# Performance work log

Hardware: AMD Instinct MI355X
Metric: run time of the kernel (lower is better)

The kernel has to match this reference:

```python
import jax, jax.numpy as jnp
import numpy as np

N = 100000
E = 1600000
C_IN = 32
HEADS = 4
C = 32          # per-head out channels
L = 3           # num layers = num_hidden_layers + 1
NEG_SLOPE = 0.2


def setup_inputs() -> dict:
    key = jax.random.key(0)
    ks = jax.random.split(key, 8)
    x = jax.random.normal(ks[0], (N, C_IN), dtype=jnp.float32)
    edge_index = jax.random.randint(ks[1], (2, E), 0, N, dtype=jnp.int64)
    edge_attr = jax.random.normal(ks[2], (E, 8), dtype=jnp.float32)  # unused by GATConv (edge_dim=None)
    scale = 1.0 / np.sqrt(C_IN)
    Ws = jax.random.normal(ks[3], (L, C_IN, HEADS * C), dtype=jnp.float32) * scale
    att_src = jax.random.normal(ks[4], (L, HEADS, C), dtype=jnp.float32) * scale
    att_dst = jax.random.normal(ks[5], (L, HEADS, C), dtype=jnp.float32) * scale
    bias = jnp.zeros((L, C), dtype=jnp.float32)
    return {"x": x, "edge_index": edge_index, "edge_attr": edge_attr,
            "Ws": Ws, "att_src": att_src, "att_dst": att_dst, "bias": bias}


def _gat_layer(x, src, dst, W, a_src, a_dst, b):
    # x: [N, C_in]; src/dst: [E'] (self-loops included); W: [C_in, H*C]
    h = (x @ W).reshape(N, HEADS, C)                      # [N, H, C]
    alpha_src = jnp.sum(h * a_src, axis=-1)               # [N, H]
    alpha_dst = jnp.sum(h * a_dst, axis=-1)               # [N, H]
    e = alpha_src[src] + alpha_dst[dst]                   # [E', H]
    e = jnp.where(e > 0, e, NEG_SLOPE * e)                # leaky_relu
    # segment softmax over incoming edges of each dst node
    m = jax.ops.segment_max(e, dst, num_segments=N)       # [N, H]
    ex = jnp.exp(e - m[dst])
    s = jax.ops.segment_sum(ex, dst, num_segments=N)      # [N, H]
    alpha = ex / (s[dst] + 1e-16)                         # [E', H]
    msg = h[src] * alpha[:, :, None]                      # [E', H, C]
    out = jax.ops.segment_sum(msg, dst, num_segments=N)   # [N, H, C]
    return out.mean(axis=1) + b                           # concat=False -> mean over heads, + bias


def reference(x, edge_index, edge_attr, Ws, att_src, att_dst, bias):
    # add self loops once (GATConv add_self_loops=True)
    loops = jnp.arange(N, dtype=edge_index.dtype)
    src = jnp.concatenate([edge_index[0], loops])
    dst = jnp.concatenate([edge_index[1], loops])
    # edge_attr unused: GATConv built without edge_dim.
    # Dropout layers are identity in eval mode.
    for l in range(L):
        x = _gat_layer(x, src, dst, Ws[l], att_src[l], att_dst[l], bias[l])
        x = jax.nn.elu(x)
    return x
```

## Files before the change

### kernel.cpp

```cpp
#include <hip/hip_runtime.h>
#include <hip/hip_bf16.h>
#include <hip/hip_fp16.h>
#include <cstdint>


__global__ void k_scan1(const int* __restrict__ deg, int n, int* __restrict__ bsums) {
    __shared__ int s[256];
    int t = threadIdx.x;
    int i = blockIdx.x * 256 + t;
    int v = (i < n) ? deg[i] : 0;
    s[t] = v; __syncthreads();
    for (int off = 128; off > 0; off >>= 1) {
        if (t < off) s[t] += s[t + off];
        __syncthreads();
    }
    if (t == 0) bsums[blockIdx.x] = s[0];
}

__global__ void k_scan2(const int* __restrict__ bsums, int nb, int* __restrict__ boffs) {
    __shared__ int s[512];
    int t = threadIdx.x;
    int v = (t < nb) ? bsums[t] : 0;
    s[t] = v; __syncthreads();
    for (int off = 1; off < 512; off <<= 1) {
        int nv = (t >= off) ? s[t - off] : 0;
        __syncthreads();
        s[t] += nv;
        __syncthreads();
    }
    if (t < nb) boffs[t] = s[t] - v;
}

__global__ void k_scan3(const int* __restrict__ deg, int n, const int* __restrict__ boffs,
                        int* __restrict__ rowst) {
    __shared__ int s[256];
    int t = threadIdx.x;
    int i = blockIdx.x * 256 + t;
    int v = (i < n) ? deg[i] : 0;
    s[t] = v; __syncthreads();
    for (int off = 1; off < 256; off <<= 1) {
        int nv = (t >= off) ? s[t - off] : 0;
        __syncthreads();
        s[t] += nv;
        __syncthreads();
    }
    int incl = s[t] + boffs[blockIdx.x];
    if (i < n) {
        rowst[i] = incl - v;
        if (i == n - 1) rowst[n] = incl;
    }
}

__global__ void k_scatter(const int* __restrict__ src, const int* __restrict__ dst,
                          const int* __restrict__ rank, const int* __restrict__ rowst,
                          int E, int* __restrict__ col) {
    int t = blockIdx.x * blockDim.x + threadIdx.x;
    int base = t * 8;
    if (base + 8 <= E) {
        int4 d[2], s[2], r[2];
#pragma unroll
        for (int k = 0; k < 2; ++k) {
            d[k] = *reinterpret_cast<const int4*>(dst + base + k * 4);
            s[k] = *reinterpret_cast<const int4*>(src + base + k * 4);
            r[k] = *reinterpret_cast<const int4*>(rank + base + k * 4);
        }
        const int* dd = reinterpret_cast<const int*>(d);
        const int* ss = reinterpret_cast<const int*>(s);
        const int* rr = reinterpret_cast<const int*>(r);
        int p[8];
#pragma unroll
        for (int k = 0; k < 8; ++k) p[k] = rowst[dd[k]] + rr[k];
#pragma unroll
        for (int k = 0; k < 8; ++k) col[p[k]] = ss[k];
    } else {
        for (int i = base; i < E; ++i) col[rowst[dst[i]] + rank[i]] = src[i];
    }
}


__device__ __forceinline__ float lane_bcast(float v, int k) {
    return __int_as_float(__builtin_amdgcn_readlane(__float_as_int(v), k));
}

__global__ void __launch_bounds__(256)
k_gemm_alpha(const float* __restrict__ x, const float* __restrict__ W,
             const float* __restrict__ a_src, const float* __restrict__ a_dst,
             __half* __restrict__ h16, float* __restrict__ alpha_src,
             float* __restrict__ alpha_dst, int n,
             const int* __restrict__ dstv, int E, int* __restrict__ deg,
             int* __restrict__ rank, int gemmBlocks) {
    if ((int)blockIdx.x >= gemmBlocks) {
        int b = blockIdx.x - gemmBlocks;
        int base = (b * 256 + threadIdx.x) * 8;
        if (base + 8 <= E) {
            int4 d[2];
#pragma unroll
            for (int k = 0; k < 2; ++k)
                d[k] = *reinterpret_cast<const int4*>(dstv + base + k * 4);
            const int* dd = reinterpret_cast<const int*>(d);
            int r[8];
#pragma unroll
            for (int k = 0; k < 8; ++k) r[k] = atomicAdd(&deg[dd[k]], 1);
#pragma unroll
            for (int k = 0; k < 2; ++k)
                *reinterpret_cast<int4*>(rank + base + k * 4) =
                    *reinterpret_cast<const int4*>(r + k * 4);
        } else {
            for (int i = base; i < E; ++i) rank[i] = atomicAdd(&deg[dstv[i]], 1);
        }
        return;
    }
    int lane = threadIdx.x & 63;
    int wave = threadIdx.x >> 6;
    int j2 = lane * 2;
    int nbase = blockIdx.x * 64 + wave * 16;

    float2 wr[32];
#pragma unroll
    for (int k = 0; k < 32; ++k)
        wr[k] = *reinterpret_cast<const float2*>(W + k * 128 + j2);
    float2 as2 = *reinterpret_cast<const float2*>(a_src + j2);
    float2 ad2 = *reinterpret_cast<const float2*>(a_dst + j2);

    float xr[16];
#pragma unroll
    for (int m = 0; m < 16; ++m) {
        int node = nbase + m;
        xr[m] = (node < n) ? x[(size_t)node * 32 + (lane & 31)] : 0.f;
    }

#pragma unroll
    for (int m = 0; m < 16; ++m) {
        int node = nbase + m;
        if (node >= n) continue;
        float acc0 = 0.f, acc1 = 0.f;
#pragma unroll
        for (int k = 0; k < 32; ++k) {
            float xv = lane_bcast(xr[m], k);
            acc0 += xv * wr[k].x;
            acc1 += xv * wr[k].y;
        }
        *reinterpret_cast<__half2*>(h16 + (size_t)node * 128 + j2) =
            __floats2half2_rn(acc0, acc1);
        float ps = acc0 * as2.x + acc1 * as2.y;
        float pd = acc0 * ad2.x + acc1 * ad2.y;
#pragma unroll
        for (int mm = 1; mm < 16; mm <<= 1) {
            ps += __shfl_xor(ps, mm, 64);
            pd += __shfl_xor(pd, mm, 64);
        }
        if ((lane & 15) == 0) {
            int head = lane >> 4;
            alpha_src[node * 4 + head] = ps;
            alpha_dst[node * 4 + head] = pd;
        }
    }
}

__device__ __forceinline__ float lrelu_exp(float e) {
    e = e > 0.f ? e : 0.2f * e;
    return __expf(e);
}

__device__ __forceinline__ float4 h16_to_f4(uint2 v) {
    float2 fa = __half22float2(*reinterpret_cast<__half2*>(&v.x));
    float2 fb = __half22float2(*reinterpret_cast<__half2*>(&v.y));
    return make_float4(fa.x, fa.y, fb.x, fb.y);
}

__global__ void k_agg(const __half* __restrict__ h16, const float* __restrict__ asrc,
                      const float* __restrict__ adst, const int* __restrict__ rowst,
                      const int* __restrict__ col, const float* __restrict__ bias,
                      float* __restrict__ out, int n) {
    int wid = (int)((blockIdx.x * (size_t)blockDim.x + threadIdx.x) >> 6);
    if (wid >= n) return;
    int lane = threadIdx.x & 63;
    int half = lane >> 5;
    int q = lane & 31;
    int head = q >> 3;
    float ad = adst[wid * 4 + head];

    float4 acc = make_float4(0.f, 0.f, 0.f, 0.f);
    float s = 0.f;
    if (half == 0) {
        float w = lrelu_exp(asrc[wid * 4 + head] + ad);
        uint2 v = *reinterpret_cast<const uint2*>(h16 + (size_t)wid * 128 + q * 4);
        float4 hv = h16_to_f4(v);
        s = w;
        acc.x = w * hv.x; acc.y = w * hv.y; acc.z = w * hv.z; acc.w = w * hv.w;
    }

    int beg = rowst[wid], end = rowst[wid + 1];
    int i = beg;
    for (; i + 8 <= end; i += 8) {
        int base = i + half * 4;
        int s0 = col[base], s1 = col[base + 1], s2 = col[base + 2], s3 = col[base + 3];
        float x0 = asrc[s0 * 4 + head];
        float x1 = asrc[s1 * 4 + head];
        float x2 = asrc[s2 * 4 + head];
        float x3 = asrc[s3 * 4 + head];
        uint2 v0 = *reinterpret_cast<const uint2*>(h16 + (size_t)s0 * 128 + q * 4);
        uint2 v1 = *reinterpret_cast<const uint2*>(h16 + (size_t)s1 * 128 + q * 4);
        uint2 v2 = *reinterpret_cast<const uint2*>(h16 + (size_t)s2 * 128 + q * 4);
        uint2 v3 = *reinterpret_cast<const uint2*>(h16 + (size_t)s3 * 128 + q * 4);
        float w0 = lrelu_exp(x0 + ad);
        float w1 = lrelu_exp(x1 + ad);
        float w2 = lrelu_exp(x2 + ad);
        float w3 = lrelu_exp(x3 + ad);
        float4 h0 = h16_to_f4(v0), h1 = h16_to_f4(v1), h2 = h16_to_f4(v2), h3 = h16_to_f4(v3);
        s += w0 + w1 + w2 + w3;
        acc.x += w0 * h0.x + w1 * h1.x + w2 * h2.x + w3 * h3.x;
        acc.y += w0 * h0.y + w1 * h1.y + w2 * h2.y + w3 * h3.y;
        acc.z += w0 * h0.z + w1 * h1.z + w2 * h2.z + w3 * h3.z;
        acc.w += w0 * h0.w + w1 * h1.w + w2 * h2.w + w3 * h3.w;
    }
    for (; i + 2 <= end; i += 2) {
        int sidx = col[i + half];
        float w = lrelu_exp(asrc[sidx * 4 + head] + ad);
        float4 hv = h16_to_f4(*reinterpret_cast<const uint2*>(h16 + (size_t)sidx * 128 + q * 4));
        s += w;
        acc.x += w * hv.x; acc.y += w * hv.y; acc.z += w * hv.z; acc.w += w * hv.w;
    }
    if (i < end && half == 0) {
        int sidx = col[i];
        float w = lrelu_exp(asrc[sidx * 4 + head] + ad);
        float4 hv = h16_to_f4(*reinterpret_cast<const uint2*>(h16 + (size_t)sidx * 128 + q * 4));
        s += w;
        acc.x += w * hv.x; acc.y += w * hv.y; acc.z += w * hv.z; acc.w += w * hv.w;
    }

    s += __shfl_xor(s, 32, 64);
    acc.x += __shfl_xor(acc.x, 32, 64);
    acc.y += __shfl_xor(acc.y, 32, 64);
    acc.z += __shfl_xor(acc.z, 32, 64);
    acc.w += __shfl_xor(acc.w, 32, 64);
    float inv = 1.f / s;
    acc.x *= inv; acc.y *= inv; acc.z *= inv; acc.w *= inv;
    acc.x += __shfl_xor(acc.x, 8, 64);  acc.x += __shfl_xor(acc.x, 16, 64);
    acc.y += __shfl_xor(acc.y, 8, 64);  acc.y += __shfl_xor(acc.y, 16, 64);
    acc.z += __shfl_xor(acc.z, 8, 64);  acc.z += __shfl_xor(acc.z, 16, 64);
    acc.w += __shfl_xor(acc.w, 8, 64);  acc.w += __shfl_xor(acc.w, 16, 64);
    if (lane < 8) {
        float4 b4 = *reinterpret_cast<const float4*>(&bias[lane * 4]);
        float o0 = acc.x * 0.25f + b4.x;
        float o1 = acc.y * 0.25f + b4.y;
        float o2 = acc.z * 0.25f + b4.z;
        float o3 = acc.w * 0.25f + b4.w;
        o0 = o0 > 0.f ? o0 : (__expf(o0) - 1.f);
        o1 = o1 > 0.f ? o1 : (__expf(o1) - 1.f);
        o2 = o2 > 0.f ? o2 : (__expf(o2) - 1.f);
        o3 = o3 > 0.f ? o3 : (__expf(o3) - 1.f);
        *reinterpret_cast<float4*>(&out[(size_t)wid * 32 + lane * 4]) =
            make_float4(o0, o1, o2, o3);
    }
}


extern "C" void kernel_launch(void* const* d_in, const int* in_sizes, int n_in,
                              void* d_out, int out_size, void* d_ws, size_t ws_size,
                              hipStream_t stream) {
    const float* x       = (const float*)d_in[0];
    const int*   ei      = (const int*)d_in[1];
    const float* Ws      = (const float*)d_in[3];
    const float* att_src = (const float*)d_in[4];
    const float* att_dst = (const float*)d_in[5];
    const float* bias    = (const float*)d_in[6];

    int N = in_sizes[0] / 32;
    int E = in_sizes[1] / 2;
    const int* srcv = ei;
    const int* dstv = ei + E;

    float* fws   = (float*)d_ws;
    __half* h16  = (__half*)fws;
    float* asrc  = (float*)(h16 + (size_t)N * 128);
    float* adst  = asrc + (size_t)N * 4;
    float* xbuf  = adst + (size_t)N * 4;
    int*   deg    = (int*)(xbuf + (size_t)N * 32);
    int*   rowst  = deg + N;
    int*   bsums  = rowst + N + 1;
    int*   boffs  = bsums + 512;
    int*   col    = boffs + 512;
    int*   rank   = col + E;

    int nb256 = (N + 255) / 256;
    int gemmBlocks = (N + 63) / 64;
    int edgeBlocks8 = (E + 8 * 256 - 1) / (8 * 256);

    hipMemsetAsync(deg, 0, (size_t)N * sizeof(int), stream);

    for (int l = 0; l < 3; ++l) {
        const float* xin = (l == 0) ? x : xbuf;
        float* xout = (l == 2) ? (float*)d_out : xbuf;
        int extra = (l == 0) ? edgeBlocks8 : 0;
        k_gemm_alpha<<<gemmBlocks + extra, 256, 0, stream>>>(
            xin, Ws + (size_t)l * 32 * 128, att_src + l * 128, att_dst + l * 128,
            h16, asrc, adst, N, dstv, E, deg, rank, gemmBlocks);
        if (l == 0) {
            k_scan1<<<nb256, 256, 0, stream>>>(deg, N, bsums);
            k_scan2<<<1, 512, 0, stream>>>(bsums, nb256, boffs);
            k_scan3<<<nb256, 256, 0, stream>>>(deg, N, boffs, rowst);
            k_scatter<<<edgeBlocks8, 256, 0, stream>>>(srcv, dstv, rank, rowst, E, col);
        }
        k_agg<<<(N + 3) / 4, 256, 0, stream>>>(
            h16, asrc, adst, rowst, col, bias + l * 32, xout, N);
    }
}
```

Baseline: 448.1 us.

## Replicate degree histogram across eight copies to spread atomic contention in CSR build

```diff
diff --git a/kernel.cpp b/kernel.cpp
--- a/kernel.cpp
+++ b/kernel.cpp
@@ -3,6 +3,21 @@
 #include <hip/hip_fp16.h>
 #include <cstdint>
 
+#define NREP 8
+
+
+__global__ void k_prefix(int* __restrict__ deg_r, int n, int* __restrict__ deg) {
+    int i = blockIdx.x * blockDim.x + threadIdx.x;
+    if (i >= n) return;
+    int sum = 0;
+#pragma unroll
+    for (int r = 0; r < NREP; ++r) {
+        int v = deg_r[r * n + i];
+        deg_r[r * n + i] = sum;
+        sum += v;
+    }
+    deg[i] = sum;
+}
 
 __global__ void k_scan1(const int* __restrict__ deg, int n, int* __restrict__ bsums) {
     __shared__ int s[256];
@@ -32,7 +47,7 @@
 }
 
 __global__ void k_scan3(const int* __restrict__ deg, int n, const int* __restrict__ boffs,
-                        int* __restrict__ rowst) {
+                        int* __restrict__ rowst, int* __restrict__ deg_r) {
     __shared__ int s[256];
     int t = threadIdx.x;
     int i = blockIdx.x * 256 + t;
@@ -46,14 +61,17 @@
     }
     int incl = s[t] + boffs[blockIdx.x];
     if (i < n) {
-        rowst[i] = incl - v;
+        int ex = incl - v;
+        rowst[i] = ex;
         if (i == n - 1) rowst[n] = incl;
+#pragma unroll
+        for (int r = 0; r < NREP; ++r) deg_r[r * n + i] += ex;
     }
 }
 
 __global__ void k_scatter(const int* __restrict__ src, const int* __restrict__ dst,
-                          const int* __restrict__ rank, const int* __restrict__ rowst,
-                          int E, int* __restrict__ col) {
+                          const int* __restrict__ rank, const int* __restrict__ deg_r,
+                          int n, int E, int* __restrict__ col) {
     int t = blockIdx.x * blockDim.x + threadIdx.x;
     int base = t * 8;
     if (base + 8 <= E) {
@@ -69,11 +87,15 @@
         const int* rr = reinterpret_cast<const int*>(r);
         int p[8];
 #pragma unroll
-        for (int k = 0; k < 8; ++k) p[k] = rowst[dd[k]] + rr[k];
+        for (int k = 0; k < 8; ++k)
+            p[k] = deg_r[(rr[k] & (NREP - 1)) * n + dd[k]] + (rr[k] >> 3);
 #pragma unroll
         for (int k = 0; k < 8; ++k) col[p[k]] = ss[k];
     } else {
-        for (int i = base; i < E; ++i) col[rowst[dst[i]] + rank[i]] = src[i];
+        for (int i = base; i < E; ++i) {
+            int rk = rank[i];
+            col[deg_r[(rk & (NREP - 1)) * n + dst[i]] + (rk >> 3)] = src[i];
+        }
     }
 }
 
@@ -87,26 +109,29 @@
              const float* __restrict__ a_src, const float* __restrict__ a_dst,
              __half* __restrict__ h16, float* __restrict__ alpha_src,
              float* __restrict__ alpha_dst, int n,
-             const int* __restrict__ dstv, int E, int* __restrict__ deg,
+             const int* __restrict__ dstv, int E, int* __restrict__ deg_r,
              int* __restrict__ rank, int gemmBlocks) {
     if ((int)blockIdx.x >= gemmBlocks) {
         int b = blockIdx.x - gemmBlocks;
-        int base = (b * 256 + threadIdx.x) * 8;
-        if (base + 8 <= E) {
-            int4 d[2];
-#pragma unroll
-            for (int k = 0; k < 2; ++k)
+        int rep = b & (NREP - 1);
+        int* degp = deg_r + (size_t)rep * n;
+        int base = (b * 256 + threadIdx.x) * 16;
+        if (base + 16 <= E) {
+            int4 d[4];
+#pragma unroll
+            for (int k = 0; k < 4; ++k)
                 d[k] = *reinterpret_cast<const int4*>(dstv + base + k * 4);
             const int* dd = reinterpret_cast<const int*>(d);
-            int r[8];
-#pragma unroll
-            for (int k = 0; k < 8; ++k) r[k] = atomicAdd(&deg[dd[k]], 1);
-#pragma unroll
-            for (int k = 0; k < 2; ++k)
+            int r[16];
+#pragma unroll
+            for (int k = 0; k < 16; ++k) r[k] = (atomicAdd(&degp[dd[k]], 1) << 3) | rep;
+#pragma unroll
+            for (int k = 0; k < 4; ++k)
                 *reinterpret_cast<int4*>(rank + base + k * 4) =
                     *reinterpret_cast<const int4*>(r + k * 4);
         } else {
-            for (int i = base; i < E; ++i) rank[i] = atomicAdd(&deg[dstv[i]], 1);
+            for (int i = base; i < E; ++i)
+                rank[i] = (atomicAdd(&degp[dstv[i]], 1) << 3) | rep;
         }
         return;
     }
@@ -276,7 +301,8 @@
     float* asrc  = (float*)(h16 + (size_t)N * 128);
     float* adst  = asrc + (size_t)N * 4;
     float* xbuf  = adst + (size_t)N * 4;
-    int*   deg    = (int*)(xbuf + (size_t)N * 32);
+    int*   deg_r  = (int*)(xbuf + (size_t)N * 32);
+    int*   deg    = deg_r + (size_t)NREP * N;
     int*   rowst  = deg + N;
     int*   bsums  = rowst + N + 1;
     int*   boffs  = bsums + 512;
@@ -285,22 +311,24 @@
 
     int nb256 = (N + 255) / 256;
     int gemmBlocks = (N + 63) / 64;
+    int histBlocks = (E + 16 * 256 - 1) / (16 * 256);
     int edgeBlocks8 = (E + 8 * 256 - 1) / (8 * 256);
 
-    hipMemsetAsync(deg, 0, (size_t)N * sizeof(int), stream);
+    hipMemsetAsync(deg_r, 0, (size_t)NREP * N * sizeof(int), stream);
 
     for (int l = 0; l < 3; ++l) {
         const float* xin = (l == 0) ? x : xbuf;
         float* xout = (l == 2) ? (float*)d_out : xbuf;
-        int extra = (l == 0) ? edgeBlocks8 : 0;
+        int extra = (l == 0) ? histBlocks : 0;
         k_gemm_alpha<<<gemmBlocks + extra, 256, 0, stream>>>(
             xin, Ws + (size_t)l * 32 * 128, att_src + l * 128, att_dst + l * 128,
-            h16, asrc, adst, N, dstv, E, deg, rank, gemmBlocks);
+            h16, asrc, adst, N, dstv, E, deg_r, rank, gemmBlocks);
         if (l == 0) {
+            k_prefix<<<nb256, 256, 0, stream>>>(deg_r, N, deg);
             k_scan1<<<nb256, 256, 0, stream>>>(deg, N, bsums);
             k_scan2<<<1, 512, 0, stream>>>(bsums, nb256, boffs);
-            k_scan3<<<nb256, 256, 0, stream>>>(deg, N, boffs, rowst);
-            k_scatter<<<edgeBlocks8, 256, 0, stream>>>(srcv, dstv, rank, rowst, E, col);
+            k_scan3<<<nb256, 256, 0, stream>>>(deg, N, boffs, rowst, deg_r);
+            k_scatter<<<edgeBlocks8, 256, 0, stream>>>(srcv, dstv, rank, deg_r, N, E, col);
         }
         k_agg<<<(N + 3) / 4, 256, 0, stream>>>(
             h16, asrc, adst, rowst, col, bias + l * 32, xout, N);
```

Result: slower. 481.1 us (+7.4%).
